# Optimization experiments

Hardware: AMD Instinct MI355X
Metric: run time of the kernel (lower is better)

## Reference

```python
import jax, jax.numpy as jnp
import numpy as np
from math import ceil, log2

N_ROWS, M_COLS = 4096, 4096
LEVELS, FILT_LEN = 8, 16


def circ_conv(a, b, n):
    # circular convolution of each row of a with filter b, both zero-padded/truncated to length n
    return jnp.fft.irfft(jnp.fft.rfft(a, n=n) * jnp.fft.rfft(b, n=n), n=n)


def forward_level(x, w):
    # one forward DWT step over rows of x using wavelet filter w
    part = x.shape[1] // 2
    g = jnp.flip(w).at[1::2].multiply(-1.0)  # scaling filter g_k = (-1)^k h_{M-k-1}
    we, wo = w[::2], w[1::2]
    ge, go = g[::2], g[1::2]
    even, odd = x[:, ::2], x[:, 1::2]
    details = circ_conv(even, we, part) + circ_conv(odd, wo, part)
    approx = circ_conv(even, ge, part) + circ_conv(odd, go, part)
    return details, approx


def backward_level(details, approx, w):
    # one inverse DWT step: zero-upsample then circular-convolve with synthesis filters
    ws = jnp.flip(w)                       # wavelet synthesis
    ss = w.at[1::2].multiply(-1.0)         # scaling synthesis
    n, md = details.shape
    fd = jnp.zeros((n, 2 * md), details.dtype).at[:, ::2].set(details)
    fa = jnp.zeros((n, 2 * approx.shape[1]), approx.dtype).at[:, ::2].set(approx)
    return circ_conv(fd, ws, 2 * md) + circ_conv(fa, ss, 2 * approx.shape[1])


def despawn(x, wavelet):
    input_length = x.shape[1]
    target = 2 ** ceil(log2(input_length))
    x = jnp.pad(x, ((0, 0), (0, target - input_length)), mode='edge')  # ReplicationPad1d
    levels = wavelet.shape[0]
    approx = x
    coeffs = []
    for lvl in range(levels):
        d, approx = forward_level(approx, wavelet[lvl])
        coeffs.append(d)
    coeffs.append(approx)
    # inverse transform (note: original applies no thresholding in forward)
    rec = coeffs[-1]
    for lvl in reversed(range(levels)):
        rec = backward_level(coeffs[lvl], rec, wavelet[lvl])
    return rec[:, :input_length], jnp.concatenate(coeffs, axis=-1)


def setup_inputs() -> dict:
    key = jax.random.key(0)
    k1, k2 = jax.random.split(key)
    inp = jax.random.normal(k1, (N_ROWS, M_COLS), dtype=jnp.float32)
    wavelet = jax.random.normal(k2, (LEVELS, FILT_LEN), dtype=jnp.float32) * 0.3
    return {"input": inp, "wavelet": wavelet}


def reference(input, wavelet):
    return despawn(input, wavelet)
```

## Files before the change

### kernel.cpp

```cpp
#include <hip/hip_runtime.h>

#define NROWS 4096
#define NCOLS 4096
#define TPB   256


__global__ __launch_bounds__(TPB, 6) void despawn_kernel(
    const float* __restrict__ in, const float* __restrict__ wv,
    float* __restrict__ out_rec, float* __restrict__ out_coef)
{
    __shared__ float P0[2048];
    __shared__ float P1[1024];
    __shared__ float Csm[512];

    const int tid = threadIdx.x;
    const int row = blockIdx.x;
    const float* rowIn = in + (size_t)row * NCOLS;
    float* crow = out_coef + (size_t)row * NCOLS;
    float* rrow = out_rec  + (size_t)row * NCOLS;

    float wl[16];

    {
        #pragma unroll
        for (int q = 0; q < 16; ++q) wl[q] = wv[q];
        float xw[32];
        const float4* X4 = (const float4*)rowIn;
        #pragma unroll
        for (int j = 0; j < 8; ++j) {
            int q = (4 * tid - 4 + j) & 1023;
            float4 v = X4[q];
            xw[4*j+0]=v.x; xw[4*j+1]=v.y; xw[4*j+2]=v.z; xw[4*j+3]=v.w;
        }
        float d[8], a[8];
        #pragma unroll
        for (int p = 0; p < 8; ++p) {
            float dd = 0.f, aa = 0.f;
            #pragma unroll
            for (int t = 0; t < 8; ++t) {
                float e = xw[16 + 2*p - 2*t];
                float o = xw[17 + 2*p - 2*t];
                dd = fmaf(wl[2*t],     e, dd);
                dd = fmaf(wl[2*t+1],   o, dd);
                aa = fmaf(wl[15-2*t],  e, aa);
                aa = fmaf(-wl[14-2*t], o, aa);
            }
            d[p] = dd; a[p] = aa;
        }
        const int k0 = tid * 8;
        ((float4*)(crow + k0))[0] = make_float4(d[0],d[1],d[2],d[3]);
        ((float4*)(crow + k0))[1] = make_float4(d[4],d[5],d[6],d[7]);
        *(float4*)(P0 + (k0>>1))        = make_float4(a[0],a[2],a[4],a[6]);
        *(float4*)(P0 + 1024 + (k0>>1)) = make_float4(a[1],a[3],a[5],a[7]);
    }
    __syncthreads();

    {
        #pragma unroll
        for (int q = 0; q < 16; ++q) wl[q] = wv[16 + q];
        const float4* E4 = (const float4*)P0;
        const float4* O4 = (const float4*)(P0 + 1024);
        float xe[12], xo[12];
        #pragma unroll
        for (int j = 0; j < 3; ++j) {
            int idx = (tid - 2 + j) & 255;
            float4 v = E4[idx], u = O4[idx];
            xe[4*j]=v.x; xe[4*j+1]=v.y; xe[4*j+2]=v.z; xe[4*j+3]=v.w;
            xo[4*j]=u.x; xo[4*j+1]=u.y; xo[4*j+2]=u.z; xo[4*j+3]=u.w;
        }
        float d[4], a[4];
        #pragma unroll
        for (int p = 0; p < 4; ++p) {
            float dd = 0.f, aa = 0.f;
            #pragma unroll
            for (int t = 0; t < 8; ++t) {
                float e = xe[8+p-t], o = xo[8+p-t];
                dd = fmaf(wl[2*t],     e, dd);
                dd = fmaf(wl[2*t+1],   o, dd);
                aa = fmaf(wl[15-2*t],  e, aa);
                aa = fmaf(-wl[14-2*t], o, aa);
            }
            d[p] = dd; a[p] = aa;
        }
        const int k0 = tid * 4;
        *(float4*)(crow + 2048 + k0) = make_float4(d[0],d[1],d[2],d[3]);
        *(float2*)(P1 + (k0>>1))       = make_float2(a[0], a[2]);
        *(float2*)(P1 + 512 + (k0>>1)) = make_float2(a[1], a[3]);
    }
    __syncthreads();

    {
        #pragma unroll
        for (int q = 0; q < 16; ++q) wl[q] = wv[32 + q];
        const float2* Ev = (const float2*)P1;
        const float2* Ov = (const float2*)(P1 + 512);
        float xe[10], xo[10];
        #pragma unroll
        for (int j = 0; j < 5; ++j) {
            int idx = (tid - 4 + j) & 255;
            float2 v = Ev[idx], u = Ov[idx];
            xe[2*j]=v.x; xe[2*j+1]=v.y;
            xo[2*j]=u.x; xo[2*j+1]=u.y;
        }
        float d[2], a[2];
        #pragma unroll
        for (int p = 0; p < 2; ++p) {
            float dd = 0.f, aa = 0.f;
            #pragma unroll
            for (int t = 0; t < 8; ++t) {
                float e = xe[8+p-t], o = xo[8+p-t];
                dd = fmaf(wl[2*t],     e, dd);
                dd = fmaf(wl[2*t+1],   o, dd);
                aa = fmaf(wl[15-2*t],  e, aa);
                aa = fmaf(-wl[14-2*t], o, aa);
            }
            d[p] = dd; a[p] = aa;
        }
        const int k0 = tid * 2;
        *(float2*)(crow + 3072 + k0) = make_float2(d[0], d[1]);
        P0[tid]       = a[0];
        P0[256 + tid] = a[1];
    }
    __syncthreads();

    {
        float* bin  = P0;
        float* bout = P1;
        int part = 256;
        int coff = 3584;
        for (int lvl = 3; lvl < 8; ++lvl) {
            #pragma unroll
            for (int q = 0; q < 16; ++q) wl[q] = wv[16*lvl + q];
            const int nth = part >> 2;
            if (tid < nth) {
                const int pm = nth - 1;
                const float4* E4 = (const float4*)bin;
                const float4* O4 = (const float4*)(bin + part);
                float xe[12], xo[12];
                #pragma unroll
                for (int j = 0; j < 3; ++j) {
                    int idx = (tid - 2 + j) & pm;
                    float4 v = E4[idx], u = O4[idx];
                    xe[4*j]=v.x; xe[4*j+1]=v.y; xe[4*j+2]=v.z; xe[4*j+3]=v.w;
                    xo[4*j]=u.x; xo[4*j+1]=u.y; xo[4*j+2]=u.z; xo[4*j+3]=u.w;
                }
                float d[4], a[4];
                #pragma unroll
                for (int p = 0; p < 4; ++p) {
                    float dd = 0.f, aa = 0.f;
                    #pragma unroll
                    for (int t = 0; t < 8; ++t) {
                        float e = xe[8+p-t], o = xo[8+p-t];
                        dd = fmaf(wl[2*t],     e, dd);
                        dd = fmaf(wl[2*t+1],   o, dd);
                        aa = fmaf(wl[15-2*t],  e, aa);
                        aa = fmaf(-wl[14-2*t], o, aa);
                    }
                    d[p] = dd; a[p] = aa;
                }
                const int k0 = tid * 4;
                float4 dv = make_float4(d[0],d[1],d[2],d[3]);
                *(float4*)(crow + coff + k0)        = dv;
                *(float4*)(Csm + (coff - 3584) + k0) = dv;
                if (lvl == 7) {
                    float4 av = make_float4(a[0],a[1],a[2],a[3]);
                    *(float4*)(crow + 4080 + k0) = av;
                    *(float4*)(Csm + 496 + k0)   = av;
                } else {
                    *(float2*)(bout + (k0>>1))              = make_float2(a[0], a[2]);
                    *(float2*)(bout + (part>>1) + (k0>>1))  = make_float2(a[1], a[3]);
                }
            }
            __syncthreads();
            float* tmp = bin; bin = bout; bout = tmp;
            coff += part;
            part >>= 1;
        }
    }

    const float* A = Csm + 496;
    {
        float* bo   = P0;
        float* balt = P1;
        int md = 16;
        int doffL = 480;
        for (int lvl = 7; lvl >= 3; --lvl) {
            #pragma unroll
            for (int q = 0; q < 16; ++q) wl[q] = wv[16*lvl + q];
            const int nth = md >> 2;
            if (tid < nth) {
                const int pm = nth - 1;
                const float4* D4 = (const float4*)(Csm + doffL);
                const float4* A4 = (const float4*)A;
                float xd[12], xa[12];
                #pragma unroll
                for (int j = 0; j < 3; ++j) {
                    int idx = (tid - 2 + j) & pm;
                    float4 v = D4[idx], u = A4[idx];
                    xd[4*j]=v.x; xd[4*j+1]=v.y; xd[4*j+2]=v.z; xd[4*j+3]=v.w;
                    xa[4*j]=u.x; xa[4*j+1]=u.y; xa[4*j+2]=u.z; xa[4*j+3]=u.w;
                }
                float r0[4], r1[4];
                #pragma unroll
                for (int p = 0; p < 4; ++p) {
                    float a0 = 0.f, a1 = 0.f;
                    #pragma unroll
                    for (int t = 0; t < 8; ++t) {
                        float dv = xd[8+p-t], av = xa[8+p-t];
                        a0 = fmaf(wl[15-2*t], dv, a0);
                        a0 = fmaf(wl[2*t],    av, a0);
                        a1 = fmaf(wl[14-2*t], dv, a1);
                        a1 = fmaf(-wl[2*t+1], av, a1);
                    }
                    r0[p] = a0; r1[p] = a1;
                }
                const int j0 = tid * 4;
                ((float4*)(bo + 2*j0))[0] = make_float4(r0[0],r1[0],r0[1],r1[1]);
                ((float4*)(bo + 2*j0))[1] = make_float4(r0[2],r1[2],r0[3],r1[3]);
            }
            __syncthreads();
            A = bo;
            float* tmp = bo; bo = balt; balt = tmp;
            md <<= 1;
            doffL -= md;
        }
    }

    {
        #pragma unroll
        for (int q = 0; q < 16; ++q) wl[q] = wv[32 + q];
        const float2* Dg = (const float2*)(crow + 3072);
        const float2* A2 = (const float2*)A;
        float xd[10], xa[10];
        #pragma unroll
        for (int j = 0; j < 5; ++j) {
            int idx = (tid - 4 + j) & 255;
            float2 v = Dg[idx], u = A2[idx];
            xd[2*j]=v.x; xd[2*j+1]=v.y;
            xa[2*j]=u.x; xa[2*j+1]=u.y;
        }
        float r0[2], r1[2];
        #pragma unroll
        for (int p = 0; p < 2; ++p) {
            float a0 = 0.f, a1 = 0.f;
            #pragma unroll
            for (int t = 0; t < 8; ++t) {
                float dv = xd[8+p-t], av = xa[8+p-t];
                a0 = fmaf(wl[15-2*t], dv, a0);
                a0 = fmaf(wl[2*t],    av, a0);
                a1 = fmaf(wl[14-2*t], dv, a1);
                a1 = fmaf(-wl[2*t+1], av, a1);
            }
            r0[p] = a0; r1[p] = a1;
        }
        const int j0 = tid * 2;
        *(float4*)(P1 + 2*j0) = make_float4(r0[0],r1[0],r0[1],r1[1]);
    }
    __syncthreads();

    {
        #pragma unroll
        for (int q = 0; q < 16; ++q) wl[q] = wv[16 + q];
        const float4* Dg = (const float4*)(crow + 2048);
        const float4* A4 = (const float4*)P1;
        float xd[12], xa[12];
        #pragma unroll
        for (int j = 0; j < 3; ++j) {
            int idx = (tid - 2 + j) & 255;
            float4 v = Dg[idx], u = A4[idx];
            xd[4*j]=v.x; xd[4*j+1]=v.y; xd[4*j+2]=v.z; xd[4*j+3]=v.w;
            xa[4*j]=u.x; xa[4*j+1]=u.y; xa[4*j+2]=u.z; xa[4*j+3]=u.w;
        }
        float r0[4], r1[4];
        #pragma unroll
        for (int p = 0; p < 4; ++p) {
            float a0 = 0.f, a1 = 0.f;
            #pragma unroll
            for (int t = 0; t < 8; ++t) {
                float dv = xd[8+p-t], av = xa[8+p-t];
                a0 = fmaf(wl[15-2*t], dv, a0);
                a0 = fmaf(wl[2*t],    av, a0);
                a1 = fmaf(wl[14-2*t], dv, a1);
                a1 = fmaf(-wl[2*t+1], av, a1);
            }
            r0[p] = a0; r1[p] = a1;
        }
        const int j0 = tid * 4;
        ((float4*)(P0 + 2*j0))[0] = make_float4(r0[0],r1[0],r0[1],r1[1]);
        ((float4*)(P0 + 2*j0))[1] = make_float4(r0[2],r1[2],r0[3],r1[3]);
    }
    __syncthreads();

    {
        #pragma unroll
        for (int q = 0; q < 16; ++q) wl[q] = wv[q];
        const float4* Dg = (const float4*)crow;
        const float4* A4 = (const float4*)P0;
        float xd[16], xa[16];
        #pragma unroll
        for (int j = 0; j < 4; ++j) {
            int idx = (2*tid - 2 + j) & 511;
            float4 v = Dg[idx], u = A4[idx];
            xd[4*j]=v.x; xd[4*j+1]=v.y; xd[4*j+2]=v.z; xd[4*j+3]=v.w;
            xa[4*j]=u.x; xa[4*j+1]=u.y; xa[4*j+2]=u.z; xa[4*j+3]=u.w;
        }
        float r0[8], r1[8];
        #pragma unroll
        for (int p = 0; p < 8; ++p) {
            float a0 = 0.f, a1 = 0.f;
            #pragma unroll
            for (int t = 0; t < 8; ++t) {
                float dv = xd[8+p-t], av = xa[8+p-t];
                a0 = fmaf(wl[15-2*t], dv, a0);
                a0 = fmaf(wl[2*t],    av, a0);
                a1 = fmaf(wl[14-2*t], dv, a1);
                a1 = fmaf(-wl[2*t+1], av, a1);
            }
            r0[p] = a0; r1[p] = a1;
        }
        const int j0 = tid * 8;
        float4* R = (float4*)(rrow + 2*j0);
        R[0] = make_float4(r0[0],r1[0],r0[1],r1[1]);
        R[1] = make_float4(r0[2],r1[2],r0[3],r1[3]);
        R[2] = make_float4(r0[4],r1[4],r0[5],r1[5]);
        R[3] = make_float4(r0[6],r1[6],r0[7],r1[7]);
    }
}

extern "C" void kernel_launch(void* const* d_in, const int* in_sizes, int n_in,
                              void* d_out, int out_size, void* d_ws, size_t ws_size,
                              hipStream_t stream) {
    (void)in_sizes; (void)n_in; (void)d_ws; (void)ws_size; (void)out_size;
    const float* in = (const float*)d_in[0];
    const float* wv = (const float*)d_in[1];
    float* out_rec  = (float*)d_out;
    float* out_coef = (float*)d_out + (size_t)NROWS * NCOLS;
    despawn_kernel<<<NROWS, TPB, 0, stream>>>(in, wv, out_rec, out_coef);
}
```

Measured before the change: 52.41 us.

## Run small DWT levels in a single wavefront and split large-level register windows

Levels 3-7 of the forward and inverse transforms now run inside one 64-thread wavefront. Block-wide __syncthreads are replaced by an LDS wait plus a scheduler barrier, and each level writes to a separate, non-aliasing region of shared memory. The first forward level and the last inverse level are split into two half-passes with smaller register windows, which lowers register pressure. The P1 buffer is enlarged and the buffer roles are reassigned. This relies on wavefront-lockstep execution for correctness within the small-level chain.

```diff
diff --git a/kernel.cpp b/kernel.cpp
--- a/kernel.cpp
+++ b/kernel.cpp
@@ -5,12 +5,63 @@
 #define TPB   256
 
 
+#define LD4(arr, base, vec) { float4 _v = (vec); (arr)[(base)] = _v.x; (arr)[(base)+1] = _v.y; (arr)[(base)+2] = _v.z; (arr)[(base)+3] = _v.w; }
+#define LD2(arr, base, vec) { float2 _v = (vec); (arr)[(base)] = _v.x; (arr)[(base)+1] = _v.y; }
+
+#define WAVE_FENCE() do { asm volatile("s_waitcnt lgkmcnt(0)" ::: "memory"); \
+                          __builtin_amdgcn_sched_barrier(0); } while (0)
+
+__device__ __forceinline__ void fwd_pt(const float* e8, const float* o8,
+                                       const float* wl, float& dd, float& aa)
+{
+    float d = 0.f, a = 0.f;
+    #pragma unroll
+    for (int t = 0; t < 8; ++t) {
+        float e = e8[-t], o = o8[-t];
+        d = fmaf(wl[2*t],     e, d);
+        d = fmaf(wl[2*t+1],   o, d);
+        a = fmaf(wl[15-2*t],  e, a);
+        a = fmaf(-wl[14-2*t], o, a);
+    }
+    dd = d; aa = a;
+}
+
+__device__ __forceinline__ void fwd_pt2(const float* e8, const float* o8,
+                                        const float* wl, float& dd, float& aa)
+{
+    float d = 0.f, a = 0.f;
+    #pragma unroll
+    for (int t = 0; t < 8; ++t) {
+        float e = e8[-2*t], o = o8[-2*t];
+        d = fmaf(wl[2*t],     e, d);
+        d = fmaf(wl[2*t+1],   o, d);
+        a = fmaf(wl[15-2*t],  e, a);
+        a = fmaf(-wl[14-2*t], o, a);
+    }
+    dd = d; aa = a;
+}
+
+__device__ __forceinline__ void bwd_pt(const float* d8, const float* a8,
+                                       const float* wl, float& rr0, float& rr1)
+{
+    float x = 0.f, y = 0.f;
+    #pragma unroll
+    for (int t = 0; t < 8; ++t) {
+        float dv = d8[-t], av = a8[-t];
+        x = fmaf(wl[15-2*t], dv, x);
+        x = fmaf(wl[2*t],    av, x);
+        y = fmaf(wl[14-2*t], dv, y);
+        y = fmaf(-wl[2*t+1], av, y);
+    }
+    rr0 = x; rr1 = y;
+}
+
 __global__ __launch_bounds__(TPB, 6) void despawn_kernel(
     const float* __restrict__ in, const float* __restrict__ wv,
     float* __restrict__ out_rec, float* __restrict__ out_coef)
 {
     __shared__ float P0[2048];
-    __shared__ float P1[1024];
+    __shared__ float P1[2048];
     __shared__ float Csm[512];
 
     const int tid = threadIdx.x;
@@ -24,34 +75,30 @@
     {
         #pragma unroll
         for (int q = 0; q < 16; ++q) wl[q] = wv[q];
-        float xw[32];
         const float4* X4 = (const float4*)rowIn;
-        #pragma unroll
-        for (int j = 0; j < 8; ++j) {
-            int q = (4 * tid - 4 + j) & 1023;
-            float4 v = X4[q];
-            xw[4*j+0]=v.x; xw[4*j+1]=v.y; xw[4*j+2]=v.z; xw[4*j+3]=v.w;
-        }
-        float d[8], a[8];
-        #pragma unroll
-        for (int p = 0; p < 8; ++p) {
-            float dd = 0.f, aa = 0.f;
-            #pragma unroll
-            for (int t = 0; t < 8; ++t) {
-                float e = xw[16 + 2*p - 2*t];
-                float o = xw[17 + 2*p - 2*t];
-                dd = fmaf(wl[2*t],     e, dd);
-                dd = fmaf(wl[2*t+1],   o, dd);
-                aa = fmaf(wl[15-2*t],  e, aa);
-                aa = fmaf(-wl[14-2*t], o, aa);
-            }
-            d[p] = dd; a[p] = aa;
-        }
         const int k0 = tid * 8;
-        ((float4*)(crow + k0))[0] = make_float4(d[0],d[1],d[2],d[3]);
-        ((float4*)(crow + k0))[1] = make_float4(d[4],d[5],d[6],d[7]);
-        *(float4*)(P0 + (k0>>1))        = make_float4(a[0],a[2],a[4],a[6]);
-        *(float4*)(P0 + 1024 + (k0>>1)) = make_float4(a[1],a[3],a[5],a[7]);
+        {
+            float xw[24];
+            #pragma unroll
+            for (int j = 0; j < 6; ++j) LD4(xw, 4*j, X4[(4*tid - 4 + j) & 1023]);
+            float d[4], a[4];
+            #pragma unroll
+            for (int p = 0; p < 4; ++p) fwd_pt2(&xw[16 + 2*p], &xw[17 + 2*p], wl, d[p], a[p]);
+            *(float4*)(crow + k0) = make_float4(d[0], d[1], d[2], d[3]);
+            *(float2*)(P0 + (k0 >> 1))        = make_float2(a[0], a[2]);
+            *(float2*)(P0 + 1024 + (k0 >> 1)) = make_float2(a[1], a[3]);
+        }
+        {
+            float xw[24];
+            #pragma unroll
+            for (int j = 0; j < 6; ++j) LD4(xw, 4*j, X4[(4*tid - 2 + j) & 1023]);
+            float d[4], a[4];
+            #pragma unroll
+            for (int p = 0; p < 4; ++p) fwd_pt2(&xw[16 + 2*p], &xw[17 + 2*p], wl, d[p], a[p]);
+            *(float4*)(crow + k0 + 4) = make_float4(d[0], d[1], d[2], d[3]);
+            *(float2*)(P0 + (k0 >> 1) + 2)        = make_float2(a[0], a[2]);
+            *(float2*)(P0 + 1024 + (k0 >> 1) + 2) = make_float2(a[1], a[3]);
+        }
     }
     __syncthreads();
 
@@ -64,28 +111,15 @@
         #pragma unroll
         for (int j = 0; j < 3; ++j) {
             int idx = (tid - 2 + j) & 255;
-            float4 v = E4[idx], u = O4[idx];
-            xe[4*j]=v.x; xe[4*j+1]=v.y; xe[4*j+2]=v.z; xe[4*j+3]=v.w;
-            xo[4*j]=u.x; xo[4*j+1]=u.y; xo[4*j+2]=u.z; xo[4*j+3]=u.w;
+            LD4(xe, 4*j, E4[idx]); LD4(xo, 4*j, O4[idx]);
         }
         float d[4], a[4];
         #pragma unroll
-        for (int p = 0; p < 4; ++p) {
-            float dd = 0.f, aa = 0.f;
-            #pragma unroll
-            for (int t = 0; t < 8; ++t) {
-                float e = xe[8+p-t], o = xo[8+p-t];
-                dd = fmaf(wl[2*t],     e, dd);
-                dd = fmaf(wl[2*t+1],   o, dd);
-                aa = fmaf(wl[15-2*t],  e, aa);
-                aa = fmaf(-wl[14-2*t], o, aa);
-            }
-            d[p] = dd; a[p] = aa;
-        }
+        for (int p = 0; p < 4; ++p) fwd_pt(&xe[8 + p], &xo[8 + p], wl, d[p], a[p]);
         const int k0 = tid * 4;
-        *(float4*)(crow + 2048 + k0) = make_float4(d[0],d[1],d[2],d[3]);
-        *(float2*)(P1 + (k0>>1))       = make_float2(a[0], a[2]);
-        *(float2*)(P1 + 512 + (k0>>1)) = make_float2(a[1], a[3]);
+        *(float4*)(crow + 2048 + k0) = make_float4(d[0], d[1], d[2], d[3]);
+        *(float2*)(P1 + (k0 >> 1))       = make_float2(a[0], a[2]);
+        *(float2*)(P1 + 512 + (k0 >> 1)) = make_float2(a[1], a[3]);
     }
     __syncthreads();
 
@@ -98,24 +132,11 @@
         #pragma unroll
         for (int j = 0; j < 5; ++j) {
             int idx = (tid - 4 + j) & 255;
-            float2 v = Ev[idx], u = Ov[idx];
-            xe[2*j]=v.x; xe[2*j+1]=v.y;
-            xo[2*j]=u.x; xo[2*j+1]=u.y;
+            LD2(xe, 2*j, Ev[idx]); LD2(xo, 2*j, Ov[idx]);
         }
         float d[2], a[2];
         #pragma unroll
-        for (int p = 0; p < 2; ++p) {
-            float dd = 0.f, aa = 0.f;
-            #pragma unroll
-            for (int t = 0; t < 8; ++t) {
-                float e = xe[8+p-t], o = xo[8+p-t];
-                dd = fmaf(wl[2*t],     e, dd);
-                dd = fmaf(wl[2*t+1],   o, dd);
-                aa = fmaf(wl[15-2*t],  e, aa);
-                aa = fmaf(-wl[14-2*t], o, aa);
-            }
-            d[p] = dd; a[p] = aa;
-        }
+        for (int p = 0; p < 2; ++p) fwd_pt(&xe[8 + p], &xo[8 + p], wl, d[p], a[p]);
         const int k0 = tid * 2;
         *(float2*)(crow + 3072 + k0) = make_float2(d[0], d[1]);
         P0[tid]       = a[0];
@@ -123,138 +144,89 @@
     }
     __syncthreads();
 
-    {
-        float* bin  = P0;
-        float* bout = P1;
-        int part = 256;
-        int coff = 3584;
+    if (tid < 64) {
+        const float* Ein = P0;
+        float* aout = P0 + 512;
+        int part = 256, cs = 0, cg = 3584;
         for (int lvl = 3; lvl < 8; ++lvl) {
             #pragma unroll
             for (int q = 0; q < 16; ++q) wl[q] = wv[16*lvl + q];
             const int nth = part >> 2;
             if (tid < nth) {
                 const int pm = nth - 1;
-                const float4* E4 = (const float4*)bin;
-                const float4* O4 = (const float4*)(bin + part);
+                const float4* E4 = (const float4*)Ein;
+                const float4* O4 = (const float4*)(Ein + part);
                 float xe[12], xo[12];
                 #pragma unroll
                 for (int j = 0; j < 3; ++j) {
                     int idx = (tid - 2 + j) & pm;
-                    float4 v = E4[idx], u = O4[idx];
-                    xe[4*j]=v.x; xe[4*j+1]=v.y; xe[4*j+2]=v.z; xe[4*j+3]=v.w;
-                    xo[4*j]=u.x; xo[4*j+1]=u.y; xo[4*j+2]=u.z; xo[4*j+3]=u.w;
+                    LD4(xe, 4*j, E4[idx]); LD4(xo, 4*j, O4[idx]);
                 }
                 float d[4], a[4];
                 #pragma unroll
-                for (int p = 0; p < 4; ++p) {
-                    float dd = 0.f, aa = 0.f;
-                    #pragma unroll
-                    for (int t = 0; t < 8; ++t) {
-                        float e = xe[8+p-t], o = xo[8+p-t];
-                        dd = fmaf(wl[2*t],     e, dd);
-                        dd = fmaf(wl[2*t+1],   o, dd);
-                        aa = fmaf(wl[15-2*t],  e, aa);
-                        aa = fmaf(-wl[14-2*t], o, aa);
-                    }
-                    d[p] = dd; a[p] = aa;
+                for (int p = 0; p < 4; ++p) fwd_pt(&xe[8 + p], &xo[8 + p], wl, d[p], a[p]);
+                const int k0 = tid * 4;
+                float4 dv = make_float4(d[0], d[1], d[2], d[3]);
+                *(float4*)(Csm + cs + k0)  = dv;
+                *(float4*)(crow + cg + k0) = dv;
+                if (lvl == 7) {
+                    float4 av = make_float4(a[0], a[1], a[2], a[3]);
+                    *(float4*)(Csm + 496 + k0)   = av;
+                    *(float4*)(crow + 4080 + k0) = av;
+                } else {
+                    *(float2*)(aout + (k0 >> 1))               = make_float2(a[0], a[2]);
+                    *(float2*)(aout + (part >> 1) + (k0 >> 1)) = make_float2(a[1], a[3]);
                 }
-                const int k0 = tid * 4;
-                float4 dv = make_float4(d[0],d[1],d[2],d[3]);
-                *(float4*)(crow + coff + k0)        = dv;
-                *(float4*)(Csm + (coff - 3584) + k0) = dv;
-                if (lvl == 7) {
-                    float4 av = make_float4(a[0],a[1],a[2],a[3]);
-                    *(float4*)(crow + 4080 + k0) = av;
-                    *(float4*)(Csm + 496 + k0)   = av;
-                } else {
-                    *(float2*)(bout + (k0>>1))              = make_float2(a[0], a[2]);
-                    *(float2*)(bout + (part>>1) + (k0>>1))  = make_float2(a[1], a[3]);
-                }
-            }
-            __syncthreads();
-            float* tmp = bin; bin = bout; bout = tmp;
-            coff += part;
-            part >>= 1;
-        }
-    }
-
-    const float* A = Csm + 496;
-    {
-        float* bo   = P0;
-        float* balt = P1;
-        int md = 16;
-        int doffL = 480;
+            }
+            WAVE_FENCE();
+            Ein = aout; aout += part; cs += part; cg += part; part >>= 1;
+        }
+        const float* A = Csm + 496;
+        float* outp = P0 + 1024;
+        int md = 16, dOff = 480;
         for (int lvl = 7; lvl >= 3; --lvl) {
             #pragma unroll
             for (int q = 0; q < 16; ++q) wl[q] = wv[16*lvl + q];
             const int nth = md >> 2;
             if (tid < nth) {
                 const int pm = nth - 1;
-                const float4* D4 = (const float4*)(Csm + doffL);
+                const float4* D4 = (const float4*)(Csm + dOff);
                 const float4* A4 = (const float4*)A;
                 float xd[12], xa[12];
                 #pragma unroll
                 for (int j = 0; j < 3; ++j) {
                     int idx = (tid - 2 + j) & pm;
-                    float4 v = D4[idx], u = A4[idx];
-                    xd[4*j]=v.x; xd[4*j+1]=v.y; xd[4*j+2]=v.z; xd[4*j+3]=v.w;
-                    xa[4*j]=u.x; xa[4*j+1]=u.y; xa[4*j+2]=u.z; xa[4*j+3]=u.w;
+                    LD4(xd, 4*j, D4[idx]); LD4(xa, 4*j, A4[idx]);
                 }
                 float r0[4], r1[4];
                 #pragma unroll
-                for (int p = 0; p < 4; ++p) {
-                    float a0 = 0.f, a1 = 0.f;
-                    #pragma unroll
-                    for (int t = 0; t < 8; ++t) {
-                        float dv = xd[8+p-t], av = xa[8+p-t];
-                        a0 = fmaf(wl[15-2*t], dv, a0);
-                        a0 = fmaf(wl[2*t],    av, a0);
-                        a1 = fmaf(wl[14-2*t], dv, a1);
-                        a1 = fmaf(-wl[2*t+1], av, a1);
-                    }
-                    r0[p] = a0; r1[p] = a1;
-                }
+                for (int p = 0; p < 4; ++p) bwd_pt(&xd[8 + p], &xa[8 + p], wl, r0[p], r1[p]);
                 const int j0 = tid * 4;
-                ((float4*)(bo + 2*j0))[0] = make_float4(r0[0],r1[0],r0[1],r1[1]);
-                ((float4*)(bo + 2*j0))[1] = make_float4(r0[2],r1[2],r0[3],r1[3]);
-            }
-            __syncthreads();
-            A = bo;
-            float* tmp = bo; bo = balt; balt = tmp;
-            md <<= 1;
-            doffL -= md;
-        }
-    }
+                ((float4*)(outp + 2*j0))[0] = make_float4(r0[0], r1[0], r0[1], r1[1]);
+                ((float4*)(outp + 2*j0))[1] = make_float4(r0[2], r1[2], r0[3], r1[3]);
+            }
+            WAVE_FENCE();
+            A = outp; outp += 2*md; md <<= 1; dOff -= md;
+        }
+    }
+    __syncthreads();
 
     {
         #pragma unroll
         for (int q = 0; q < 16; ++q) wl[q] = wv[32 + q];
         const float2* Dg = (const float2*)(crow + 3072);
-        const float2* A2 = (const float2*)A;
+        const float2* Av = (const float2*)(P0 + 1504);
         float xd[10], xa[10];
         #pragma unroll
         for (int j = 0; j < 5; ++j) {
             int idx = (tid - 4 + j) & 255;
-            float2 v = Dg[idx], u = A2[idx];
-            xd[2*j]=v.x; xd[2*j+1]=v.y;
-            xa[2*j]=u.x; xa[2*j+1]=u.y;
+            LD2(xd, 2*j, Dg[idx]); LD2(xa, 2*j, Av[idx]);
         }
         float r0[2], r1[2];
         #pragma unroll
-        for (int p = 0; p < 2; ++p) {
-            float a0 = 0.f, a1 = 0.f;
-            #pragma unroll
-            for (int t = 0; t < 8; ++t) {
-                float dv = xd[8+p-t], av = xa[8+p-t];
-                a0 = fmaf(wl[15-2*t], dv, a0);
-                a0 = fmaf(wl[2*t],    av, a0);
-                a1 = fmaf(wl[14-2*t], dv, a1);
-                a1 = fmaf(-wl[2*t+1], av, a1);
-            }
-            r0[p] = a0; r1[p] = a1;
-        }
+        for (int p = 0; p < 2; ++p) bwd_pt(&xd[8 + p], &xa[8 + p], wl, r0[p], r1[p]);
         const int j0 = tid * 2;
-        *(float4*)(P1 + 2*j0) = make_float4(r0[0],r1[0],r0[1],r1[1]);
+        *(float4*)(P0 + 2*j0) = make_float4(r0[0], r1[0], r0[1], r1[1]);
     }
     __syncthreads();
 
@@ -262,32 +234,19 @@
         #pragma unroll
         for (int q = 0; q < 16; ++q) wl[q] = wv[16 + q];
         const float4* Dg = (const float4*)(crow + 2048);
-        const float4* A4 = (const float4*)P1;
+        const float4* Av = (const float4*)P0;
         float xd[12], xa[12];
         #pragma unroll
         for (int j = 0; j < 3; ++j) {
             int idx = (tid - 2 + j) & 255;
-            float4 v = Dg[idx], u = A4[idx];
-            xd[4*j]=v.x; xd[4*j+1]=v.y; xd[4*j+2]=v.z; xd[4*j+3]=v.w;
-            xa[4*j]=u.x; xa[4*j+1]=u.y; xa[4*j+2]=u.z; xa[4*j+3]=u.w;
+            LD4(xd, 4*j, Dg[idx]); LD4(xa, 4*j, Av[idx]);
         }
         float r0[4], r1[4];
         #pragma unroll
-        for (int p = 0; p < 4; ++p) {
-            float a0 = 0.f, a1 = 0.f;
-            #pragma unroll
-            for (int t = 0; t < 8; ++t) {
-                float dv = xd[8+p-t], av = xa[8+p-t];
-                a0 = fmaf(wl[15-2*t], dv, a0);
-                a0 = fmaf(wl[2*t],    av, a0);
-                a1 = fmaf(wl[14-2*t], dv, a1);
-                a1 = fmaf(-wl[2*t+1], av, a1);
-            }
-            r0[p] = a0; r1[p] = a1;
-        }
+        for (int p = 0; p < 4; ++p) bwd_pt(&xd[8 + p], &xa[8 + p], wl, r0[p], r1[p]);
         const int j0 = tid * 4;
-        ((float4*)(P0 + 2*j0))[0] = make_float4(r0[0],r1[0],r0[1],r1[1]);
-        ((float4*)(P0 + 2*j0))[1] = make_float4(r0[2],r1[2],r0[3],r1[3]);
+        ((float4*)(P1 + 2*j0))[0] = make_float4(r0[0], r1[0], r0[1], r1[1]);
+        ((float4*)(P1 + 2*j0))[1] = make_float4(r0[2], r1[2], r0[3], r1[3]);
     }
     __syncthreads();
 
@@ -295,35 +254,34 @@
         #pragma unroll
         for (int q = 0; q < 16; ++q) wl[q] = wv[q];
         const float4* Dg = (const float4*)crow;
-        const float4* A4 = (const float4*)P0;
-        float xd[16], xa[16];
-        #pragma unroll
-        for (int j = 0; j < 4; ++j) {
-            int idx = (2*tid - 2 + j) & 511;
-            float4 v = Dg[idx], u = A4[idx];
-            xd[4*j]=v.x; xd[4*j+1]=v.y; xd[4*j+2]=v.z; xd[4*j+3]=v.w;
-            xa[4*j]=u.x; xa[4*j+1]=u.y; xa[4*j+2]=u.z; xa[4*j+3]=u.w;
-        }
-        float r0[8], r1[8];
-        #pragma unroll
-        for (int p = 0; p < 8; ++p) {
-            float a0 = 0.f, a1 = 0.f;
-            #pragma unroll
-            for (int t = 0; t < 8; ++t) {
-                float dv = xd[8+p-t], av = xa[8+p-t];
-                a0 = fmaf(wl[15-2*t], dv, a0);
-                a0 = fmaf(wl[2*t],    av, a0);
-                a1 = fmaf(wl[14-2*t], dv, a1);
-                a1 = fmaf(-wl[2*t+1], av, a1);
-            }
-            r0[p] = a0; r1[p] = a1;
-        }
+        const float4* Av = (const float4*)P1;
         const int j0 = tid * 8;
-        float4* R = (float4*)(rrow + 2*j0);
-        R[0] = make_float4(r0[0],r1[0],r0[1],r1[1]);
-        R[1] = make_float4(r0[2],r1[2],r0[3],r1[3]);
-        R[2] = make_float4(r0[4],r1[4],r0[5],r1[5]);
-        R[3] = make_float4(r0[6],r1[6],r0[7],r1[7]);
+        {
+            float xd[12], xa[12];
+            #pragma unroll
+            for (int c = 0; c < 3; ++c) {
+                int idx = (2*tid - 2 + c) & 511;
+                LD4(xd, 4*c, Dg[idx]); LD4(xa, 4*c, Av[idx]);
+            }
+            float r0[4], r1[4];
+            #pragma unroll
+            for (int p = 0; p < 4; ++p) bwd_pt(&xd[8 + p], &xa[8 + p], wl, r0[p], r1[p]);
+            ((float4*)(rrow + 2*j0))[0] = make_float4(r0[0], r1[0], r0[1], r1[1]);
+            ((float4*)(rrow + 2*j0))[1] = make_float4(r0[2], r1[2], r0[3], r1[3]);
+        }
+        {
+            float xd[12], xa[12];
+            #pragma unroll
+            for (int c = 0; c < 3; ++c) {
+                int idx = (2*tid - 1 + c) & 511;
+                LD4(xd, 4*c, Dg[idx]); LD4(xa, 4*c, Av[idx]);
+            }
+            float r0[4], r1[4];
+            #pragma unroll
+            for (int p = 0; p < 4; ++p) bwd_pt(&xd[8 + p], &xa[8 + p], wl, r0[p], r1[p]);
+            ((float4*)(rrow + 2*j0))[2] = make_float4(r0[0], r1[0], r0[1], r1[1]);
+            ((float4*)(rrow + 2*j0))[3] = make_float4(r0[2], r1[2], r0[3], r1[3]);
+        }
     }
 }
 
```

Result: slower. 56.83 us (+8.4%).
